# Kernel optimization log

Hardware: AMD Instinct MI355X
Metric: run time of the kernel (lower is better)

The kernel has to match this reference:

```python
import jax, jax.numpy as jnp
import numpy as np

N = 100000   # nodes
E = 1600000  # edges (avg degree 16)
D_IN = 128
HID = [128, 128]
D_OUT = 1


def _linear_params(key, in_c, out_c):
    k1, k2 = jax.random.split(key)
    s = 1.0 / np.sqrt(in_c)
    w = jax.random.uniform(k1, (out_c, in_c), jnp.float32, -s, s)
    b = jax.random.uniform(k2, (out_c,), jnp.float32, -s, s)
    return w, b


def setup_inputs() -> dict:
    key = jax.random.key(0)
    ks = jax.random.split(key, 16)
    inp = {}
    inp["x"] = jax.random.normal(ks[0], (N, D_IN), jnp.float32)
    inp["edge_index"] = jax.random.randint(ks[1], (2, E), 0, N, jnp.int32)
    # 3 GINConvs: dims (128->128), (128->128), (128->128); each MLP = Linear, ReLU, Linear
    dims = [(D_IN, HID[0]), (HID[0], HID[1]), (HID[1], HID[1])]
    for i, (ic, oc) in enumerate(dims):
        k1, k2 = jax.random.split(ks[2 + i])
        w1, b1 = _linear_params(k1, ic, oc)
        w2, b2 = _linear_params(k2, oc, oc)
        inp[f"c{i}_w1"], inp[f"c{i}_b1"] = w1, b1
        inp[f"c{i}_w2"], inp[f"c{i}_b2"] = w2, b2
        inp[f"c{i}_eps"] = jnp.zeros((), jnp.float32)  # train_eps=True, init 0
    last = HID[-1]
    inp["fc1_w"], inp["fc1_b"] = _linear_params(ks[8], last, last // 2)
    inp["fc2_w"], inp["fc2_b"] = _linear_params(ks[9], last // 2, D_OUT)
    return inp


def reference(x, edge_index,
              c0_w1, c0_b1, c0_w2, c0_b2, c0_eps,
              c1_w1, c1_b1, c1_w2, c1_b2, c1_eps,
              c2_w1, c2_b1, c2_w2, c2_b2, c2_eps,
              fc1_w, fc1_b, fc2_w, fc2_b):
    src, dst = edge_index[0], edge_index[1]  # messages flow src -> dst
    n = x.shape[0]

    def gin_conv(h, w1, b1, w2, b2, eps):
        # sum-aggregate neighbor features: scatter-add h[src] into dst
        agg = jax.ops.segment_sum(h[src], dst, num_segments=n)
        z = (1.0 + eps) * h + agg
        z = jax.nn.relu(z @ w1.T + b1) @ w2.T + b2  # GIN MLP
        return jax.nn.relu(z)  # outer ReLU in GINNet.forward

    h = gin_conv(x, c0_w1, c0_b1, c0_w2, c0_b2, c0_eps)
    h = gin_conv(h, c1_w1, c1_b1, c1_w2, c1_b2, c1_eps)
    h = gin_conv(h, c2_w1, c2_b1, c2_w2, c2_b2, c2_eps)
    h = jax.nn.relu(h @ fc1_w.T + fc1_b)
    return jax.nn.sigmoid(h @ fc2_w.T + fc2_b)
```

## Files before the change

### kernel.cpp

```cpp
#include <hip/hip_runtime.h>
#include <math.h>


using f16   = _Float16;
using f16x4 = __attribute__((ext_vector_type(4))) _Float16;
using f16x8 = __attribute__((ext_vector_type(8))) _Float16;
using f32x4 = __attribute__((ext_vector_type(4))) float;

constexpr int BINBLK = 256;

__device__ inline void glds16(const void* g, void* l) {
    __builtin_amdgcn_global_load_lds(
        (const __attribute__((address_space(1))) void*)g,
        (__attribute__((address_space(3))) void*)l, 16, 0, 0);
}


__global__ __launch_bounds__(512) void bucket_count_kernel(const int* __restrict__ dst,
                                                           int* __restrict__ cntM,
                                                           int E, int nbuck) {
    __shared__ int cnt[512];
    for (int i = threadIdx.x; i < nbuck; i += 512) cnt[i] = 0;
    __syncthreads();
    int chunk = (E + gridDim.x - 1) / gridDim.x;
    int lo = blockIdx.x * chunk, hi = min(lo + chunk, E);
    for (int e = lo + threadIdx.x; e < hi; e += 512)
        atomicAdd(&cnt[dst[e] >> 8], 1);
    __syncthreads();
    for (int i = threadIdx.x; i < nbuck; i += 512)
        cntM[(size_t)i * gridDim.x + blockIdx.x] = cnt[i];
}

__global__ __launch_bounds__(256) void scan_partial(const int* __restrict__ deg,
                                                    int* __restrict__ bsum, int n) {
    __shared__ int red[256];
    int b = blockIdx.x, t = threadIdx.x;
    int base = b * 1024;
    int s = 0;
#pragma unroll
    for (int j = 0; j < 4; ++j) {
        int idx = base + j * 256 + t;
        if (idx < n) s += deg[idx];
    }
    red[t] = s;
    __syncthreads();
    for (int d = 128; d > 0; d >>= 1) {
        if (t < d) red[t] += red[t + d];
        __syncthreads();
    }
    if (t == 0) bsum[b] = red[0];
}

__global__ __launch_bounds__(128) void scan_bsum(const int* __restrict__ bsum,
                                                 int* __restrict__ bbase, int nb,
                                                 int* __restrict__ total_out) {
    __shared__ int s[128];
    int t = threadIdx.x;
    s[t] = (t < nb) ? bsum[t] : 0;
    __syncthreads();
    for (int d = 1; d < 128; d <<= 1) {
        int v = (t >= d) ? s[t - d] : 0;
        __syncthreads();
        s[t] += v;
        __syncthreads();
    }
    bbase[t] = (t > 0) ? s[t - 1] : 0;
    if (t == 127) total_out[0] = s[127];
}

__global__ __launch_bounds__(256) void scan_final(const int* __restrict__ deg,
                                                  const int* __restrict__ bbase,
                                                  int* __restrict__ outA,
                                                  int* __restrict__ outB, int n) {
    __shared__ int red[256];
    int b = blockIdx.x, t = threadIdx.x;
    int base = b * 1024 + t * 4;
    int d0 = 0, d1 = 0, d2 = 0, d3 = 0;
    if (base + 3 < n) {
        int4 v = *(const int4*)&deg[base];
        d0 = v.x; d1 = v.y; d2 = v.z; d3 = v.w;
    } else {
        if (base < n) d0 = deg[base];
        if (base + 1 < n) d1 = deg[base + 1];
        if (base + 2 < n) d2 = deg[base + 2];
    }
    red[t] = d0 + d1 + d2 + d3;
    __syncthreads();
    for (int d = 1; d < 256; d <<= 1) {
        int v = (t >= d) ? red[t - d] : 0;
        __syncthreads();
        red[t] += v;
        __syncthreads();
    }
    int ex = bbase[b] + ((t > 0) ? red[t - 1] : 0);
    int o0 = ex, o1 = ex + d0, o2 = o1 + d1, o3 = o2 + d2;
    if (base + 3 < n) {
        *(int4*)&outA[base] = make_int4(o0, o1, o2, o3);
        *(int4*)&outB[base] = make_int4(o0, o1, o2, o3);
    } else {
        if (base < n) { outA[base] = o0; outB[base] = o0; }
        if (base + 1 < n) { outA[base + 1] = o1; outB[base + 1] = o1; }
        if (base + 2 < n) { outA[base + 2] = o2; outB[base + 2] = o2; }
    }
}

__global__ __launch_bounds__(512) void bin_kernel(const int* __restrict__ src,
                                                  const int* __restrict__ dst,
                                                  const int* __restrict__ baseM,
                                                  int2* __restrict__ stage, int E, int nbuck) {
    __shared__ int cur[512];
    for (int i = threadIdx.x; i < nbuck; i += 512)
        cur[i] = baseM[(size_t)i * gridDim.x + blockIdx.x];
    __syncthreads();
    int chunk = (E + gridDim.x - 1) / gridDim.x;
    int lo = blockIdx.x * chunk, hi = min(lo + chunk, E);
    for (int e = lo + threadIdx.x; e < hi; e += 512) {
        int d = dst[e];
        int p = atomicAdd(&cur[d >> 8], 1);
        stage[p] = make_int2(src[e], d);
    }
}

__global__ __launch_bounds__(256) void csr_kernel(const int2* __restrict__ stage,
                                                  const int* __restrict__ baseM,
                                                  int* __restrict__ offs,
                                                  int* __restrict__ col,
                                                  int E, int N, int nbuck, int binblk) {
    constexpr int CAP = 10240;
    __shared__ int cnt[256];
    __shared__ int sc[256];
    __shared__ int colbuf[CAP];
    int b = blockIdx.x, t = threadIdx.x;
    int base = baseM[(size_t)b * binblk];
    int end = (b + 1 < nbuck) ? baseM[(size_t)(b + 1) * binblk] : E;
    cnt[t] = 0;
    __syncthreads();
    for (int e = base + t; e < end; e += 256)
        atomicAdd(&cnt[stage[e].y & 255], 1);
    __syncthreads();
    int myCnt = cnt[t];
    sc[t] = myCnt;
    __syncthreads();
    for (int d = 1; d < 256; d <<= 1) {
        int u = (t >= d) ? sc[t - d] : 0;
        __syncthreads();
        sc[t] += u;
        __syncthreads();
    }
    int myExcl = sc[t] - myCnt;
    int node = b * 256 + t;
    if (node <= N) offs[node] = base + myExcl;
    cnt[t] = myExcl;
    __syncthreads();
    for (int e = base + t; e < end; e += 256) {
        int2 sd = stage[e];
        int p = atomicAdd(&cnt[sd.y & 255], 1);
        if (p < CAP) colbuf[p] = sd.x;
        else col[base + p] = sd.x;
    }
    __syncthreads();
    int lim = min(end - base, CAP);
    for (int i = t; i < lim; i += 256) col[base + i] = colbuf[i];
}

__global__ void cvt4_kernel(const float* __restrict__ in, f16* __restrict__ out, int nq) {
    int stride = gridDim.x * blockDim.x;
    for (int i = blockIdx.x * blockDim.x + threadIdx.x; i < nq; i += stride) {
        float4 v = *(const float4*)(in + (size_t)i * 4);
        f16x4 o = {(f16)v.x, (f16)v.y, (f16)v.z, (f16)v.w};
        *(f16x4*)(out + (size_t)i * 4) = o;
    }
}

struct CvtPack {
    const float* s[7];
    f16* d[7];
    int nq[7];
};
__global__ void cvt_pack_kernel(CvtPack p) {
    int seg = blockIdx.y;
    int nq = p.nq[seg];
    const float* in = p.s[seg];
    f16* out = p.d[seg];
    int stride = gridDim.x * blockDim.x;
    for (int i = blockIdx.x * blockDim.x + threadIdx.x; i < nq; i += stride) {
        float4 v = *(const float4*)(in + (size_t)i * 4);
        f16x4 o = {(f16)v.x, (f16)v.y, (f16)v.z, (f16)v.w};
        *(f16x4*)(out + (size_t)i * 4) = o;
    }
}

__global__ __launch_bounds__(256) void agg_kernel(const f16* __restrict__ h,
                                                  const int* __restrict__ offs,
                                                  const int* __restrict__ col,
                                                  const float* __restrict__ epsp,
                                                  f16* __restrict__ z, int n) {
    int node = blockIdx.x * 8 + (threadIdx.x >> 5);
    int li = threadIdx.x & 31;
    bool valid = node < n;
    int nd = valid ? node : (n - 1);
    const f16x4* hp = (const f16x4*)h;
    float e1 = 1.0f + epsp[0];
    f16x4 self = hp[(size_t)nd * 32 + li];
    float a0 = (float)self.x * e1, a1 = (float)self.y * e1;
    float a2 = (float)self.z * e1, a3 = (float)self.w * e1;
    int lo = offs[nd], hi = valid ? offs[nd + 1] : lo;

    int e = lo;
    for (; e + 8 <= hi; e += 8) {
        int idx[8];
#pragma unroll
        for (int j = 0; j < 8; ++j) idx[j] = col[e + j];
        f16x4 v[8];
#pragma unroll
        for (int j = 0; j < 8; ++j) v[j] = hp[(size_t)idx[j] * 32 + li];
#pragma unroll
        for (int j = 0; j < 8; ++j) {
            a0 += (float)v[j].x; a1 += (float)v[j].y;
            a2 += (float)v[j].z; a3 += (float)v[j].w;
        }
    }
    if (e + 4 <= hi) {
        int idx[4];
#pragma unroll
        for (int j = 0; j < 4; ++j) idx[j] = col[e + j];
        f16x4 v[4];
#pragma unroll
        for (int j = 0; j < 4; ++j) v[j] = hp[(size_t)idx[j] * 32 + li];
#pragma unroll
        for (int j = 0; j < 4; ++j) {
            a0 += (float)v[j].x; a1 += (float)v[j].y;
            a2 += (float)v[j].z; a3 += (float)v[j].w;
        }
        e += 4;
    }
    for (; e < hi; ++e) {
        f16x4 v = hp[(size_t)col[e] * 32 + li];
        a0 += (float)v.x; a1 += (float)v.y; a2 += (float)v.z; a3 += (float)v.w;
    }
    if (valid) {
        f16x4 o = {(f16)a0, (f16)a1, (f16)a2, (f16)a3};
        __builtin_nontemporal_store(o, (f16x4*)z + (size_t)nd * 32 + li);
    }
}

template <bool LAST>
__global__ __launch_bounds__(256) void conv_mlp_kernel(
    const f16* __restrict__ Z, const f16* __restrict__ W1f,
    const float* __restrict__ b1, const f16* __restrict__ W2f,
    const float* __restrict__ b2, f16* __restrict__ Hout, int M,
    const f16* __restrict__ fc1wf, const float* __restrict__ fc1b,
    const float* __restrict__ fc2w, const float* __restrict__ fc2b,
    float* __restrict__ out) {
    __shared__ __align__(16) f16 As[128 * 128];
    __shared__ __align__(16) f16 Ws[128 * 128];
    __shared__ float Red[LAST ? 128 * 17 : 1];

    const int tid = threadIdx.x;
    const int w = tid >> 6, lane = tid & 63;
    const int frow = lane & 15, kgrp = lane >> 4;
    const int m0 = blockIdx.x * 128;
    const int u = lane & 15, rsub = lane >> 4;

#pragma unroll
    for (int i = 0; i < 8; ++i) {
        int rowbase = (w * 8 + i) * 4;
        int r = rowbase + rsub;
        int gr = m0 + r;
        if (gr >= M) gr = M - 1;
        glds16(Z + (size_t)gr * 128 + ((u ^ (r & 7)) << 3), &As[rowbase * 128]);
    }
#pragma unroll
    for (int i = 0; i < 8; ++i) {
        int rowbase = (w * 8 + i) * 4;
        int r = rowbase + rsub;
        glds16(W1f + (size_t)r * 128 + ((u ^ (r & 7)) << 3), &Ws[rowbase * 128]);
    }
    __syncthreads();

    const int arow0 = w * 32 + frow;
    f32x4 acc[2][8];
#pragma unroll
    for (int mi = 0; mi < 2; ++mi)
#pragma unroll
        for (int nj = 0; nj < 8; ++nj) acc[mi][nj] = (f32x4){0.f, 0.f, 0.f, 0.f};

#pragma unroll
    for (int kk = 0; kk < 4; ++kk) {
        int kb = kk * 4 + kgrp;
        f16x8 a[2], b[8];
#pragma unroll
        for (int mi = 0; mi < 2; ++mi) {
            int r = arow0 + mi * 16;
            a[mi] = *(const f16x8*)&As[r * 128 + ((kb ^ (r & 7)) << 3)];
        }
#pragma unroll
        for (int nj = 0; nj < 8; ++nj) {
            int r = nj * 16 + frow;
            b[nj] = *(const f16x8*)&Ws[r * 128 + ((kb ^ (r & 7)) << 3)];
        }
#pragma unroll
        for (int mi = 0; mi < 2; ++mi)
#pragma unroll
            for (int nj = 0; nj < 8; ++nj)
                acc[mi][nj] = __builtin_amdgcn_mfma_f32_16x16x32_f16(a[mi], b[nj],
                                                                     acc[mi][nj], 0, 0, 0);
    }
    __syncthreads();

#pragma unroll
    for (int i = 0; i < 8; ++i) {
        int rowbase = (w * 8 + i) * 4;
        int r = rowbase + rsub;
        glds16(W2f + (size_t)r * 128 + ((u ^ (r & 7)) << 3), &Ws[rowbase * 128]);
    }
    {
        float bv[8];
#pragma unroll
        for (int nj = 0; nj < 8; ++nj) bv[nj] = b1[nj * 16 + frow];
#pragma unroll
        for (int mi = 0; mi < 2; ++mi)
#pragma unroll
            for (int nj = 0; nj < 8; ++nj) {
                int row0 = w * 32 + mi * 16 + kgrp * 4;
                int c = nj * 16 + frow;
                int cu = c >> 3, cl = c & 7;
#pragma unroll
                for (int r = 0; r < 4; ++r) {
                    int rr = row0 + r;
                    As[rr * 128 + ((cu ^ (rr & 7)) << 3) + cl] =
                        (f16)fmaxf(acc[mi][nj][r] + bv[nj], 0.f);
                }
            }
    }
    __syncthreads();

#pragma unroll
    for (int mi = 0; mi < 2; ++mi)
#pragma unroll
        for (int nj = 0; nj < 8; ++nj) acc[mi][nj] = (f32x4){0.f, 0.f, 0.f, 0.f};
#pragma unroll
    for (int kk = 0; kk < 4; ++kk) {
        int kb = kk * 4 + kgrp;
        f16x8 a[2], b[8];
#pragma unroll
        for (int mi = 0; mi < 2; ++mi) {
            int r = arow0 + mi * 16;
            a[mi] = *(const f16x8*)&As[r * 128 + ((kb ^ (r & 7)) << 3)];
        }
#pragma unroll
        for (int nj = 0; nj < 8; ++nj) {
            int r = nj * 16 + frow;
            b[nj] = *(const f16x8*)&Ws[r * 128 + ((kb ^ (r & 7)) << 3)];
        }
#pragma unroll
        for (int mi = 0; mi < 2; ++mi)
#pragma unroll
            for (int nj = 0; nj < 8; ++nj)
                acc[mi][nj] = __builtin_amdgcn_mfma_f32_16x16x32_f16(a[mi], b[nj],
                                                                     acc[mi][nj], 0, 0, 0);
    }

    float bv2[8];
#pragma unroll
    for (int nj = 0; nj < 8; ++nj) bv2[nj] = b2[nj * 16 + frow];

    if (!LAST) {
        __syncthreads();
#pragma unroll
        for (int mi = 0; mi < 2; ++mi)
#pragma unroll
            for (int nj = 0; nj < 8; ++nj) {
                int row0 = w * 32 + mi * 16 + kgrp * 4;
                int c = nj * 16 + frow;
#pragma unroll
                for (int r = 0; r < 4; ++r)
                    As[(row0 + r) * 128 + c] = (f16)fmaxf(acc[mi][nj][r] + bv2[nj], 0.f);
            }
        __syncthreads();
        for (int idx = tid; idx < 128 * 16; idx += 256) {
            int r = idx >> 4, q = idx & 15;
            int gm = m0 + r;
            if (gm < M)
                *(float4*)(Hout + (size_t)gm * 128 + q * 8) = *(const float4*)&As[r * 128 + q * 8];
        }
    } else {
        __syncthreads();
#pragma unroll
        for (int i = 0; i < 4; ++i) {
            int rowbase = (w * 4 + i) * 4;
            int r = rowbase + rsub;
            glds16(fc1wf + (size_t)r * 128 + ((u ^ (r & 7)) << 3), &Ws[rowbase * 128]);
        }
#pragma unroll
        for (int mi = 0; mi < 2; ++mi)
#pragma unroll
            for (int nj = 0; nj < 8; ++nj) {
                int row0 = w * 32 + mi * 16 + kgrp * 4;
                int c = nj * 16 + frow;
                int cu = c >> 3, cl = c & 7;
#pragma unroll
                for (int r = 0; r < 4; ++r) {
                    int rr = row0 + r;
                    As[rr * 128 + ((cu ^ (rr & 7)) << 3) + cl] =
                        (f16)fmaxf(acc[mi][nj][r] + bv2[nj], 0.f);
                }
            }
        __syncthreads();

        f32x4 acc3[2][4];
#pragma unroll
        for (int mi = 0; mi < 2; ++mi)
#pragma unroll
            for (int nj = 0; nj < 4; ++nj) acc3[mi][nj] = (f32x4){0.f, 0.f, 0.f, 0.f};
#pragma unroll
        for (int kk = 0; kk < 4; ++kk) {
            int kb = kk * 4 + kgrp;
            f16x8 a[2], b[4];
#pragma unroll
            for (int mi = 0; mi < 2; ++mi) {
                int r = arow0 + mi * 16;
                a[mi] = *(const f16x8*)&As[r * 128 + ((kb ^ (r & 7)) << 3)];
            }
#pragma unroll
            for (int nj = 0; nj < 4; ++nj) {
                int r = nj * 16 + frow;
                b[nj] = *(const f16x8*)&Ws[r * 128 + ((kb ^ (r & 7)) << 3)];
            }
#pragma unroll
            for (int mi = 0; mi < 2; ++mi)
#pragma unroll
                for (int nj = 0; nj < 4; ++nj)
                    acc3[mi][nj] = __builtin_amdgcn_mfma_f32_16x16x32_f16(a[mi], b[nj],
                                                                          acc3[mi][nj], 0, 0, 0);
        }
        float bvf[4], f2[4];
#pragma unroll
        for (int nj = 0; nj < 4; ++nj) {
            bvf[nj] = fc1b[nj * 16 + frow];
            f2[nj] = fc2w[nj * 16 + frow];
        }
        float part[2][4];
#pragma unroll
        for (int mi = 0; mi < 2; ++mi)
#pragma unroll
            for (int r = 0; r < 4; ++r) part[mi][r] = 0.f;
#pragma unroll
        for (int mi = 0; mi < 2; ++mi)
#pragma unroll
            for (int nj = 0; nj < 4; ++nj)
#pragma unroll
                for (int r = 0; r < 4; ++r)
                    part[mi][r] += fmaxf(acc3[mi][nj][r] + bvf[nj], 0.f) * f2[nj];
#pragma unroll
        for (int mi = 0; mi < 2; ++mi)
#pragma unroll
            for (int r = 0; r < 4; ++r)
                Red[(w * 32 + mi * 16 + kgrp * 4 + r) * 17 + frow] = part[mi][r];
        __syncthreads();
        if (tid < 128) {
            float s = fc2b[0];
#pragma unroll
            for (int q = 0; q < 16; ++q) s += Red[tid * 17 + q];
            int m = m0 + tid;
            if (m < M) out[m] = 1.f / (1.f + expf(-s));
        }
    }
}

extern "C" void kernel_launch(void* const* d_in, const int* in_sizes, int n_in,
                              void* d_out, int out_size, void* d_ws, size_t ws_size,
                              hipStream_t stream) {
    const float* x = (const float*)d_in[0];
    const int* ei = (const int*)d_in[1];
    const int N = in_sizes[0] / 128;
    const int E = in_sizes[1] / 2;
    const int* srcIdx = ei;
    const int* dstIdx = ei + E;

    const float* w1[3] = {(const float*)d_in[2], (const float*)d_in[7], (const float*)d_in[12]};
    const float* b1[3] = {(const float*)d_in[3], (const float*)d_in[8], (const float*)d_in[13]};
    const float* w2[3] = {(const float*)d_in[4], (const float*)d_in[9], (const float*)d_in[14]};
    const float* b2[3] = {(const float*)d_in[5], (const float*)d_in[10], (const float*)d_in[15]};
    const float* eps[3] = {(const float*)d_in[6], (const float*)d_in[11], (const float*)d_in[16]};
    const float* fc1w = (const float*)d_in[17];
    const float* fc1b = (const float*)d_in[18];
    const float* fc2w = (const float*)d_in[19];
    const float* fc2b = (const float*)d_in[20];

    char* ws = (char*)d_ws;
    size_t p = 0;
    auto carve = [&](size_t bytes) -> char* {
        char* r = ws + p;
        p = (p + bytes + 255) & ~(size_t)255;
        return r;
    };
    const int nbuck = (N + 255) >> 8;
    const int nm = nbuck * BINBLK;
    int* offs = (int*)carve((size_t)(N + 1) * 4);
    int* col = (int*)carve((size_t)E * 4);
    int* cntM = (int*)carve((size_t)nm * 4);
    int* baseM = (int*)carve((size_t)nm * 4);
    int* baseM2 = (int*)carve((size_t)nm * 4);
    int* bsum = (int*)carve(128 * 4);
    int* bbase = (int*)carve(128 * 4);
    int* tot = (int*)carve(4);
    int2* stage = (int2*)carve((size_t)E * 8);
    f16* H0 = (f16*)carve((size_t)N * 128 * 2);
    f16* H1 = (f16*)carve((size_t)N * 128 * 2);
    f16* Z = (f16*)carve((size_t)N * 128 * 2);
    f16* w1f[3], *w2f[3];
    for (int i = 0; i < 3; ++i) {
        w1f[i] = (f16*)carve(128 * 128 * 2);
        w2f[i] = (f16*)carve(128 * 128 * 2);
    }
    f16* fc1wf = (f16*)carve(64 * 128 * 2);
    (void)ws_size;

    const int SB2 = (nm + 1023) / 1024;
    bucket_count_kernel<<<BINBLK, 512, 0, stream>>>(dstIdx, cntM, E, nbuck);
    scan_partial<<<SB2, 256, 0, stream>>>(cntM, bsum, nm);
    scan_bsum<<<1, 128, 0, stream>>>(bsum, bbase, SB2, tot);
    scan_final<<<SB2, 256, 0, stream>>>(cntM, bbase, baseM, baseM2, nm);
    bin_kernel<<<BINBLK, 512, 0, stream>>>(srcIdx, dstIdx, baseM, stage, E, nbuck);
    csr_kernel<<<nbuck, 256, 0, stream>>>(stage, baseM, offs, col, E, N, nbuck, BINBLK);

    cvt4_kernel<<<2048, 256, 0, stream>>>(x, H0, N * 128 / 4);
    CvtPack cp;
    for (int i = 0; i < 3; ++i) {
        cp.s[i] = w1[i];     cp.d[i] = w1f[i];     cp.nq[i] = 128 * 128 / 4;
        cp.s[3 + i] = w2[i]; cp.d[3 + i] = w2f[i]; cp.nq[3 + i] = 128 * 128 / 4;
    }
    cp.s[6] = fc1w; cp.d[6] = fc1wf; cp.nq[6] = 64 * 128 / 4;
    cvt_pack_kernel<<<dim3(16, 7), 256, 0, stream>>>(cp);

    const int aggGrid = (N + 7) / 8;
    const int gemmGrid = (N + 127) / 128;

    agg_kernel<<<aggGrid, 256, 0, stream>>>(H0, offs, col, eps[0], Z, N);
    conv_mlp_kernel<false><<<gemmGrid, 256, 0, stream>>>(
        Z, w1f[0], b1[0], w2f[0], b2[0], H1, N, nullptr, nullptr, nullptr, nullptr, nullptr);
    agg_kernel<<<aggGrid, 256, 0, stream>>>(H1, offs, col, eps[1], Z, N);
    conv_mlp_kernel<false><<<gemmGrid, 256, 0, stream>>>(
        Z, w1f[1], b1[1], w2f[1], b2[1], H0, N, nullptr, nullptr, nullptr, nullptr, nullptr);
    agg_kernel<<<aggGrid, 256, 0, stream>>>(H0, offs, col, eps[2], Z, N);
    conv_mlp_kernel<true><<<gemmGrid, 256, 0, stream>>>(
        Z, w1f[2], b1[2], w2f[2], b2[2], nullptr, N, fc1wf, fc1b, fc2w, fc2b, (float*)d_out);
}
```

Measured before the change: 299.9 us.

## Fuse neighbor aggregation into GIN MLP kernel with LDS-staged CSR columns

Removes the separate aggregation kernel and the Z intermediate buffer. Each 512-thread block now gathers and sums neighbor features for its 128 nodes directly into shared memory, then runs the two-layer MLP on that tile. Nodes are handed out to 8-lane groups through a shared-memory atomic counter for load balance. The block's CSR column slice is staged in LDS when it fits, and each wave now computes 16 rows instead of 32. This saves the Z write and read plus launch overhead, at the cost of higher LDS use per block and the gather no longer overlapping with the GEMM phase across blocks.

```diff
diff --git a/kernel.cpp b/kernel.cpp
--- a/kernel.cpp
+++ b/kernel.cpp
@@ -190,71 +190,24 @@
     }
 }
 
-__global__ __launch_bounds__(256) void agg_kernel(const f16* __restrict__ h,
-                                                  const int* __restrict__ offs,
-                                                  const int* __restrict__ col,
-                                                  const float* __restrict__ epsp,
-                                                  f16* __restrict__ z, int n) {
-    int node = blockIdx.x * 8 + (threadIdx.x >> 5);
-    int li = threadIdx.x & 31;
-    bool valid = node < n;
-    int nd = valid ? node : (n - 1);
-    const f16x4* hp = (const f16x4*)h;
-    float e1 = 1.0f + epsp[0];
-    f16x4 self = hp[(size_t)nd * 32 + li];
-    float a0 = (float)self.x * e1, a1 = (float)self.y * e1;
-    float a2 = (float)self.z * e1, a3 = (float)self.w * e1;
-    int lo = offs[nd], hi = valid ? offs[nd + 1] : lo;
-
-    int e = lo;
-    for (; e + 8 <= hi; e += 8) {
-        int idx[8];
-#pragma unroll
-        for (int j = 0; j < 8; ++j) idx[j] = col[e + j];
-        f16x4 v[8];
-#pragma unroll
-        for (int j = 0; j < 8; ++j) v[j] = hp[(size_t)idx[j] * 32 + li];
-#pragma unroll
-        for (int j = 0; j < 8; ++j) {
-            a0 += (float)v[j].x; a1 += (float)v[j].y;
-            a2 += (float)v[j].z; a3 += (float)v[j].w;
-        }
-    }
-    if (e + 4 <= hi) {
-        int idx[4];
-#pragma unroll
-        for (int j = 0; j < 4; ++j) idx[j] = col[e + j];
-        f16x4 v[4];
-#pragma unroll
-        for (int j = 0; j < 4; ++j) v[j] = hp[(size_t)idx[j] * 32 + li];
-#pragma unroll
-        for (int j = 0; j < 4; ++j) {
-            a0 += (float)v[j].x; a1 += (float)v[j].y;
-            a2 += (float)v[j].z; a3 += (float)v[j].w;
-        }
-        e += 4;
-    }
-    for (; e < hi; ++e) {
-        f16x4 v = hp[(size_t)col[e] * 32 + li];
-        a0 += (float)v.x; a1 += (float)v.y; a2 += (float)v.z; a3 += (float)v.w;
-    }
-    if (valid) {
-        f16x4 o = {(f16)a0, (f16)a1, (f16)a2, (f16)a3};
-        __builtin_nontemporal_store(o, (f16x4*)z + (size_t)nd * 32 + li);
-    }
-}
-
 template <bool LAST>
-__global__ __launch_bounds__(256) void conv_mlp_kernel(
-    const f16* __restrict__ Z, const f16* __restrict__ W1f,
-    const float* __restrict__ b1, const f16* __restrict__ W2f,
-    const float* __restrict__ b2, f16* __restrict__ Hout, int M,
+__global__ __launch_bounds__(512, 4) void conv_fused_kernel(
+    const f16* __restrict__ H, const int* __restrict__ offs,
+    const int* __restrict__ col, const float* __restrict__ epsp,
+    const f16* __restrict__ W1f, const float* __restrict__ b1,
+    const f16* __restrict__ W2f, const float* __restrict__ b2,
+    f16* __restrict__ Hout, int M,
     const f16* __restrict__ fc1wf, const float* __restrict__ fc1b,
     const float* __restrict__ fc2w, const float* __restrict__ fc2b,
     float* __restrict__ out) {
+    constexpr int COLCAP = 2560;
     __shared__ __align__(16) f16 As[128 * 128];
     __shared__ __align__(16) f16 Ws[128 * 128];
-    __shared__ float Red[LAST ? 128 * 17 : 1];
+    __shared__ __align__(16) int poolB[COLCAP + 132];
+    int* colLDS = poolB;
+    int* sOffs = poolB + COLCAP;
+    int* ctr = poolB + COLCAP + 130;
+    float* Red = (float*)poolB;
 
     const int tid = threadIdx.x;
     const int w = tid >> 6, lane = tid & 63;
@@ -263,54 +216,116 @@
     const int u = lane & 15, rsub = lane >> 4;
 
 #pragma unroll
-    for (int i = 0; i < 8; ++i) {
-        int rowbase = (w * 8 + i) * 4;
-        int r = rowbase + rsub;
-        int gr = m0 + r;
-        if (gr >= M) gr = M - 1;
-        glds16(Z + (size_t)gr * 128 + ((u ^ (r & 7)) << 3), &As[rowbase * 128]);
-    }
-#pragma unroll
-    for (int i = 0; i < 8; ++i) {
-        int rowbase = (w * 8 + i) * 4;
+    for (int i = 0; i < 4; ++i) {
+        int rowbase = (w * 4 + i) * 4;
         int r = rowbase + rsub;
         glds16(W1f + (size_t)r * 128 + ((u ^ (r & 7)) << 3), &Ws[rowbase * 128]);
     }
-    __syncthreads();
-
-    const int arow0 = w * 32 + frow;
-    f32x4 acc[2][8];
-#pragma unroll
-    for (int mi = 0; mi < 2; ++mi)
-#pragma unroll
-        for (int nj = 0; nj < 8; ++nj) acc[mi][nj] = (f32x4){0.f, 0.f, 0.f, 0.f};
-
+    for (int i = tid; i < 129; i += 512) sOffs[i] = offs[min(m0 + i, M)];
+    if (tid == 0) *ctr = 0;
+    __syncthreads();
+    const int cbase = sOffs[0];
+    const int wlen = sOffs[128] - cbase;
+    const bool useLds = wlen <= COLCAP;
+    if (useLds)
+        for (int i = tid; i < wlen; i += 512)
+            colLDS[i] = __builtin_nontemporal_load(&col[cbase + i]);
+    __syncthreads();
+
+    {
+        const int li = tid & 7;
+        const int gbase = lane & ~7;
+        const f16x8* hp = (const f16x8*)H;
+        const float e1 = 1.0f + epsp[0];
+        for (;;) {
+            int n = 0;
+            if (li == 0) n = atomicAdd(ctr, 1);
+            n = __shfl(n, gbase, 64);
+            if (n >= 128) break;
+            const int coA = li, coB = li + 8;
+            f16* dstA = &As[n * 128 + ((coA ^ (n & 7)) << 3)];
+            f16* dstB = &As[n * 128 + ((coB ^ (n & 7)) << 3)];
+            const int node = m0 + n;
+            if (node >= M) {
+                f16x8 zz = {};
+                *(f16x8*)dstA = zz;
+                *(f16x8*)dstB = zz;
+                continue;
+            }
+            f16x8 sA = hp[(size_t)node * 16 + coA];
+            f16x8 sB = hp[(size_t)node * 16 + coB];
+            float a[8], b[8];
+#pragma unroll
+            for (int c = 0; c < 8; ++c) {
+                a[c] = (float)sA[c] * e1;
+                b[c] = (float)sB[c] * e1;
+            }
+            int lo = sOffs[n] - cbase, hi = sOffs[n + 1] - cbase;
+            int e = lo;
+            for (; e + 6 <= hi; e += 6) {
+                int idx[6];
+#pragma unroll
+                for (int j = 0; j < 6; ++j)
+                    idx[j] = useLds ? colLDS[e + j] : col[cbase + e + j];
+                f16x8 vA[6], vB[6];
+#pragma unroll
+                for (int j = 0; j < 6; ++j) {
+                    vA[j] = hp[(size_t)idx[j] * 16 + coA];
+                    vB[j] = hp[(size_t)idx[j] * 16 + coB];
+                }
+#pragma unroll
+                for (int j = 0; j < 6; ++j)
+#pragma unroll
+                    for (int c = 0; c < 8; ++c) {
+                        a[c] += (float)vA[j][c];
+                        b[c] += (float)vB[j][c];
+                    }
+            }
+            for (; e < hi; ++e) {
+                int idx = useLds ? colLDS[e] : col[cbase + e];
+                f16x8 vA = hp[(size_t)idx * 16 + coA];
+                f16x8 vB = hp[(size_t)idx * 16 + coB];
+#pragma unroll
+                for (int c = 0; c < 8; ++c) {
+                    a[c] += (float)vA[c];
+                    b[c] += (float)vB[c];
+                }
+            }
+            f16x8 oA, oB;
+#pragma unroll
+            for (int c = 0; c < 8; ++c) {
+                oA[c] = (f16)a[c];
+                oB[c] = (f16)b[c];
+            }
+            *(f16x8*)dstA = oA;
+            *(f16x8*)dstB = oB;
+        }
+    }
+    __syncthreads();
+
+    const int arow0 = w * 16 + frow;
+    f32x4 acc[8];
+#pragma unroll
+    for (int nj = 0; nj < 8; ++nj) acc[nj] = (f32x4){0.f, 0.f, 0.f, 0.f};
 #pragma unroll
     for (int kk = 0; kk < 4; ++kk) {
         int kb = kk * 4 + kgrp;
-        f16x8 a[2], b[8];
-#pragma unroll
-        for (int mi = 0; mi < 2; ++mi) {
-            int r = arow0 + mi * 16;
-            a[mi] = *(const f16x8*)&As[r * 128 + ((kb ^ (r & 7)) << 3)];
-        }
+        f16x8 a = *(const f16x8*)&As[arow0 * 128 + ((kb ^ (arow0 & 7)) << 3)];
+        f16x8 b[8];
 #pragma unroll
         for (int nj = 0; nj < 8; ++nj) {
             int r = nj * 16 + frow;
             b[nj] = *(const f16x8*)&Ws[r * 128 + ((kb ^ (r & 7)) << 3)];
         }
 #pragma unroll
-        for (int mi = 0; mi < 2; ++mi)
-#pragma unroll
-            for (int nj = 0; nj < 8; ++nj)
-                acc[mi][nj] = __builtin_amdgcn_mfma_f32_16x16x32_f16(a[mi], b[nj],
-                                                                     acc[mi][nj], 0, 0, 0);
-    }
-    __syncthreads();
-
-#pragma unroll
-    for (int i = 0; i < 8; ++i) {
-        int rowbase = (w * 8 + i) * 4;
+        for (int nj = 0; nj < 8; ++nj)
+            acc[nj] = __builtin_amdgcn_mfma_f32_16x16x32_f16(a, b[nj], acc[nj], 0, 0, 0);
+    }
+    __syncthreads();
+
+#pragma unroll
+    for (int i = 0; i < 4; ++i) {
+        int rowbase = (w * 4 + i) * 4;
         int r = rowbase + rsub;
         glds16(W2f + (size_t)r * 128 + ((u ^ (r & 7)) << 3), &Ws[rowbase * 128]);
     }
@@ -318,67 +333,53 @@
         float bv[8];
 #pragma unroll
         for (int nj = 0; nj < 8; ++nj) bv[nj] = b1[nj * 16 + frow];
-#pragma unroll
-        for (int mi = 0; mi < 2; ++mi)
-#pragma unroll
-            for (int nj = 0; nj < 8; ++nj) {
-                int row0 = w * 32 + mi * 16 + kgrp * 4;
-                int c = nj * 16 + frow;
-                int cu = c >> 3, cl = c & 7;
-#pragma unroll
-                for (int r = 0; r < 4; ++r) {
-                    int rr = row0 + r;
-                    As[rr * 128 + ((cu ^ (rr & 7)) << 3) + cl] =
-                        (f16)fmaxf(acc[mi][nj][r] + bv[nj], 0.f);
-                }
-            }
-    }
-    __syncthreads();
-
-#pragma unroll
-    for (int mi = 0; mi < 2; ++mi)
-#pragma unroll
-        for (int nj = 0; nj < 8; ++nj) acc[mi][nj] = (f32x4){0.f, 0.f, 0.f, 0.f};
+        const int row0 = w * 16 + kgrp * 4;
+#pragma unroll
+        for (int nj = 0; nj < 8; ++nj) {
+            int c = nj * 16 + frow;
+            int cu = c >> 3, cl = c & 7;
+#pragma unroll
+            for (int r = 0; r < 4; ++r) {
+                int rr = row0 + r;
+                As[rr * 128 + ((cu ^ (rr & 7)) << 3) + cl] =
+                    (f16)fmaxf(acc[nj][r] + bv[nj], 0.f);
+            }
+        }
+    }
+    __syncthreads();
+
+#pragma unroll
+    for (int nj = 0; nj < 8; ++nj) acc[nj] = (f32x4){0.f, 0.f, 0.f, 0.f};
 #pragma unroll
     for (int kk = 0; kk < 4; ++kk) {
         int kb = kk * 4 + kgrp;
-        f16x8 a[2], b[8];
-#pragma unroll
-        for (int mi = 0; mi < 2; ++mi) {
-            int r = arow0 + mi * 16;
-            a[mi] = *(const f16x8*)&As[r * 128 + ((kb ^ (r & 7)) << 3)];
-        }
+        f16x8 a = *(const f16x8*)&As[arow0 * 128 + ((kb ^ (arow0 & 7)) << 3)];
+        f16x8 b[8];
 #pragma unroll
         for (int nj = 0; nj < 8; ++nj) {
             int r = nj * 16 + frow;
             b[nj] = *(const f16x8*)&Ws[r * 128 + ((kb ^ (r & 7)) << 3)];
         }
 #pragma unroll
-        for (int mi = 0; mi < 2; ++mi)
-#pragma unroll
-            for (int nj = 0; nj < 8; ++nj)
-                acc[mi][nj] = __builtin_amdgcn_mfma_f32_16x16x32_f16(a[mi], b[nj],
-                                                                     acc[mi][nj], 0, 0, 0);
-    }
-
+        for (int nj = 0; nj < 8; ++nj)
+            acc[nj] = __builtin_amdgcn_mfma_f32_16x16x32_f16(a, b[nj], acc[nj], 0, 0, 0);
+    }
     float bv2[8];
 #pragma unroll
     for (int nj = 0; nj < 8; ++nj) bv2[nj] = b2[nj * 16 + frow];
 
     if (!LAST) {
         __syncthreads();
-#pragma unroll
-        for (int mi = 0; mi < 2; ++mi)
-#pragma unroll
-            for (int nj = 0; nj < 8; ++nj) {
-                int row0 = w * 32 + mi * 16 + kgrp * 4;
-                int c = nj * 16 + frow;
-#pragma unroll
-                for (int r = 0; r < 4; ++r)
-                    As[(row0 + r) * 128 + c] = (f16)fmaxf(acc[mi][nj][r] + bv2[nj], 0.f);
-            }
-        __syncthreads();
-        for (int idx = tid; idx < 128 * 16; idx += 256) {
+        const int row0 = w * 16 + kgrp * 4;
+#pragma unroll
+        for (int nj = 0; nj < 8; ++nj) {
+            int c = nj * 16 + frow;
+#pragma unroll
+            for (int r = 0; r < 4; ++r)
+                As[(row0 + r) * 128 + c] = (f16)fmaxf(acc[nj][r] + bv2[nj], 0.f);
+        }
+        __syncthreads();
+        for (int idx = tid; idx < 128 * 16; idx += 512) {
             int r = idx >> 4, q = idx & 15;
             int gm = m0 + r;
             if (gm < M)
@@ -387,52 +388,41 @@
     } else {
         __syncthreads();
 #pragma unroll
-        for (int i = 0; i < 4; ++i) {
-            int rowbase = (w * 4 + i) * 4;
+        for (int i = 0; i < 2; ++i) {
+            int rowbase = (w * 2 + i) * 4;
             int r = rowbase + rsub;
             glds16(fc1wf + (size_t)r * 128 + ((u ^ (r & 7)) << 3), &Ws[rowbase * 128]);
         }
-#pragma unroll
-        for (int mi = 0; mi < 2; ++mi)
-#pragma unroll
-            for (int nj = 0; nj < 8; ++nj) {
-                int row0 = w * 32 + mi * 16 + kgrp * 4;
-                int c = nj * 16 + frow;
-                int cu = c >> 3, cl = c & 7;
-#pragma unroll
-                for (int r = 0; r < 4; ++r) {
-                    int rr = row0 + r;
-                    As[rr * 128 + ((cu ^ (rr & 7)) << 3) + cl] =
-                        (f16)fmaxf(acc[mi][nj][r] + bv2[nj], 0.f);
-                }
-            }
-        __syncthreads();
-
-        f32x4 acc3[2][4];
-#pragma unroll
-        for (int mi = 0; mi < 2; ++mi)
-#pragma unroll
-            for (int nj = 0; nj < 4; ++nj) acc3[mi][nj] = (f32x4){0.f, 0.f, 0.f, 0.f};
+        const int row0 = w * 16 + kgrp * 4;
+#pragma unroll
+        for (int nj = 0; nj < 8; ++nj) {
+            int c = nj * 16 + frow;
+            int cu = c >> 3, cl = c & 7;
+#pragma unroll
+            for (int r = 0; r < 4; ++r) {
+                int rr = row0 + r;
+                As[rr * 128 + ((cu ^ (rr & 7)) << 3) + cl] =
+                    (f16)fmaxf(acc[nj][r] + bv2[nj], 0.f);
+            }
+        }
+        __syncthreads();
+
+        f32x4 acc3[4];
+#pragma unroll
+        for (int nj = 0; nj < 4; ++nj) acc3[nj] = (f32x4){0.f, 0.f, 0.f, 0.f};
 #pragma unroll
         for (int kk = 0; kk < 4; ++kk) {
             int kb = kk * 4 + kgrp;
-            f16x8 a[2], b[4];
-#pragma unroll
-            for (int mi = 0; mi < 2; ++mi) {
-                int r = arow0 + mi * 16;
-                a[mi] = *(const f16x8*)&As[r * 128 + ((kb ^ (r & 7)) << 3)];
-            }
+            f16x8 a = *(const f16x8*)&As[arow0 * 128 + ((kb ^ (arow0 & 7)) << 3)];
+            f16x8 b[4];
 #pragma unroll
             for (int nj = 0; nj < 4; ++nj) {
                 int r = nj * 16 + frow;
                 b[nj] = *(const f16x8*)&Ws[r * 128 + ((kb ^ (r & 7)) << 3)];
             }
 #pragma unroll
-            for (int mi = 0; mi < 2; ++mi)
-#pragma unroll
-                for (int nj = 0; nj < 4; ++nj)
-                    acc3[mi][nj] = __builtin_amdgcn_mfma_f32_16x16x32_f16(a[mi], b[nj],
-                                                                          acc3[mi][nj], 0, 0, 0);
+            for (int nj = 0; nj < 4; ++nj)
+                acc3[nj] = __builtin_amdgcn_mfma_f32_16x16x32_f16(a, b[nj], acc3[nj], 0, 0, 0);
         }
         float bvf[4], f2[4];
 #pragma unroll
@@ -440,23 +430,14 @@
             bvf[nj] = fc1b[nj * 16 + frow];
             f2[nj] = fc2w[nj * 16 + frow];
         }
-        float part[2][4];
-#pragma unroll
-        for (int mi = 0; mi < 2; ++mi)
-#pragma unroll
-            for (int r = 0; r < 4; ++r) part[mi][r] = 0.f;
-#pragma unroll
-        for (int mi = 0; mi < 2; ++mi)
-#pragma unroll
-            for (int nj = 0; nj < 4; ++nj)
-#pragma unroll
-                for (int r = 0; r < 4; ++r)
-                    part[mi][r] += fmaxf(acc3[mi][nj][r] + bvf[nj], 0.f) * f2[nj];
-#pragma unroll
-        for (int mi = 0; mi < 2; ++mi)
+        float part[4] = {0.f, 0.f, 0.f, 0.f};
+#pragma unroll
+        for (int nj = 0; nj < 4; ++nj)
 #pragma unroll
             for (int r = 0; r < 4; ++r)
-                Red[(w * 32 + mi * 16 + kgrp * 4 + r) * 17 + frow] = part[mi][r];
+                part[r] += fmaxf(acc3[nj][r] + bvf[nj], 0.f) * f2[nj];
+#pragma unroll
+        for (int r = 0; r < 4; ++r) Red[(row0 + r) * 17 + frow] = part[r];
         __syncthreads();
         if (tid < 128) {
             float s = fc2b[0];
@@ -508,7 +489,6 @@
     int2* stage = (int2*)carve((size_t)E * 8);
     f16* H0 = (f16*)carve((size_t)N * 128 * 2);
     f16* H1 = (f16*)carve((size_t)N * 128 * 2);
-    f16* Z = (f16*)carve((size_t)N * 128 * 2);
     f16* w1f[3], *w2f[3];
     for (int i = 0; i < 3; ++i) {
         w1f[i] = (f16*)carve(128 * 128 * 2);
@@ -534,16 +514,15 @@
     cp.s[6] = fc1w; cp.d[6] = fc1wf; cp.nq[6] = 64 * 128 / 4;
     cvt_pack_kernel<<<dim3(16, 7), 256, 0, stream>>>(cp);
 
-    const int aggGrid = (N + 7) / 8;
     const int gemmGrid = (N + 127) / 128;
 
-    agg_kernel<<<aggGrid, 256, 0, stream>>>(H0, offs, col, eps[0], Z, N);
-    conv_mlp_kernel<false><<<gemmGrid, 256, 0, stream>>>(
-        Z, w1f[0], b1[0], w2f[0], b2[0], H1, N, nullptr, nullptr, nullptr, nullptr, nullptr);
-    agg_kernel<<<aggGrid, 256, 0, stream>>>(H1, offs, col, eps[1], Z, N);
-    conv_mlp_kernel<false><<<gemmGrid, 256, 0, stream>>>(
-        Z, w1f[1], b1[1], w2f[1], b2[1], H0, N, nullptr, nullptr, nullptr, nullptr, nullptr);
-    agg_kernel<<<aggGrid, 256, 0, stream>>>(H0, offs, col, eps[2], Z, N);
-    conv_mlp_kernel<true><<<gemmGrid, 256, 0, stream>>>(
-        Z, w1f[2], b1[2], w2f[2], b2[2], nullptr, N, fc1wf, fc1b, fc2w, fc2b, (float*)d_out);
-}
+    conv_fused_kernel<false><<<gemmGrid, 512, 0, stream>>>(
+        H0, offs, col, eps[0], w1f[0], b1[0], w2f[0], b2[0], H1, N,
+        nullptr, nullptr, nullptr, nullptr, nullptr);
+    conv_fused_kernel<false><<<gemmGrid, 512, 0, stream>>>(
+        H1, offs, col, eps[1], w1f[1], b1[1], w2f[1], b2[1], H0, N,
+        nullptr, nullptr, nullptr, nullptr, nullptr);
+    conv_fused_kernel<true><<<gemmGrid, 512, 0, stream>>>(
+        H0, offs, col, eps[2], w1f[2], b1[2], w2f[2], b2[2], nullptr, N,
+        fc1wf, fc1b, fc2w, fc2b, (float*)d_out);
+}
```

Result: slower. 315.6 us (+5.2%).

## Restructure aggregation with LDS-staged column indices and shrink CSR staging

Applied to the files above, without the earlier changes.

The aggregation kernel now processes 128 nodes per block. It preloads the block's column indices into LDS and hands nodes to 8-lane groups through an LDS atomic counter, with each lane loading 16-byte f16x8 vectors. The aim is to cut repeated global index loads, balance work across nodes of different degree, and widen the gather loads. The CSR build also packs src and the low dst byte into one int, which halves staging traffic, and drops the duplicate baseM2 output. The packing assumes source indices fit in 24 bits, and the dynamic counter adds some atomic overhead.

```diff
diff --git a/kernel.cpp b/kernel.cpp
--- a/kernel.cpp
+++ b/kernel.cpp
@@ -70,8 +70,7 @@
 
 __global__ __launch_bounds__(256) void scan_final(const int* __restrict__ deg,
                                                   const int* __restrict__ bbase,
-                                                  int* __restrict__ outA,
-                                                  int* __restrict__ outB, int n) {
+                                                  int* __restrict__ outA, int n) {
     __shared__ int red[256];
     int b = blockIdx.x, t = threadIdx.x;
     int base = b * 1024 + t * 4;
@@ -96,18 +95,17 @@
     int o0 = ex, o1 = ex + d0, o2 = o1 + d1, o3 = o2 + d2;
     if (base + 3 < n) {
         *(int4*)&outA[base] = make_int4(o0, o1, o2, o3);
-        *(int4*)&outB[base] = make_int4(o0, o1, o2, o3);
     } else {
-        if (base < n) { outA[base] = o0; outB[base] = o0; }
-        if (base + 1 < n) { outA[base + 1] = o1; outB[base + 1] = o1; }
-        if (base + 2 < n) { outA[base + 2] = o2; outB[base + 2] = o2; }
+        if (base < n) outA[base] = o0;
+        if (base + 1 < n) outA[base + 1] = o1;
+        if (base + 2 < n) outA[base + 2] = o2;
     }
 }
 
 __global__ __launch_bounds__(512) void bin_kernel(const int* __restrict__ src,
                                                   const int* __restrict__ dst,
                                                   const int* __restrict__ baseM,
-                                                  int2* __restrict__ stage, int E, int nbuck) {
+                                                  int* __restrict__ stage, int E, int nbuck) {
     __shared__ int cur[512];
     for (int i = threadIdx.x; i < nbuck; i += 512)
         cur[i] = baseM[(size_t)i * gridDim.x + blockIdx.x];
@@ -117,11 +115,11 @@
     for (int e = lo + threadIdx.x; e < hi; e += 512) {
         int d = dst[e];
         int p = atomicAdd(&cur[d >> 8], 1);
-        stage[p] = make_int2(src[e], d);
-    }
-}
-
-__global__ __launch_bounds__(256) void csr_kernel(const int2* __restrict__ stage,
+        stage[p] = (src[e] << 8) | (d & 255);
+    }
+}
+
+__global__ __launch_bounds__(256) void csr_kernel(const int* __restrict__ stage,
                                                   const int* __restrict__ baseM,
                                                   int* __restrict__ offs,
                                                   int* __restrict__ col,
@@ -136,7 +134,7 @@
     cnt[t] = 0;
     __syncthreads();
     for (int e = base + t; e < end; e += 256)
-        atomicAdd(&cnt[stage[e].y & 255], 1);
+        atomicAdd(&cnt[stage[e] & 255], 1);
     __syncthreads();
     int myCnt = cnt[t];
     sc[t] = myCnt;
@@ -153,10 +151,10 @@
     cnt[t] = myExcl;
     __syncthreads();
     for (int e = base + t; e < end; e += 256) {
-        int2 sd = stage[e];
-        int p = atomicAdd(&cnt[sd.y & 255], 1);
-        if (p < CAP) colbuf[p] = sd.x;
-        else col[base + p] = sd.x;
+        int sd = stage[e];
+        int p = atomicAdd(&cnt[sd & 255], 1);
+        if (p < CAP) colbuf[p] = sd >> 8;
+        else col[base + p] = sd >> 8;
     }
     __syncthreads();
     int lim = min(end - base, CAP);
@@ -195,52 +193,83 @@
                                                   const int* __restrict__ col,
                                                   const float* __restrict__ epsp,
                                                   f16* __restrict__ z, int n) {
-    int node = blockIdx.x * 8 + (threadIdx.x >> 5);
-    int li = threadIdx.x & 31;
-    bool valid = node < n;
-    int nd = valid ? node : (n - 1);
-    const f16x4* hp = (const f16x4*)h;
-    float e1 = 1.0f + epsp[0];
-    f16x4 self = hp[(size_t)nd * 32 + li];
-    float a0 = (float)self.x * e1, a1 = (float)self.y * e1;
-    float a2 = (float)self.z * e1, a3 = (float)self.w * e1;
-    int lo = offs[nd], hi = valid ? offs[nd + 1] : lo;
-
-    int e = lo;
-    for (; e + 8 <= hi; e += 8) {
-        int idx[8];
-#pragma unroll
-        for (int j = 0; j < 8; ++j) idx[j] = col[e + j];
-        f16x4 v[8];
-#pragma unroll
-        for (int j = 0; j < 8; ++j) v[j] = hp[(size_t)idx[j] * 32 + li];
-#pragma unroll
-        for (int j = 0; j < 8; ++j) {
-            a0 += (float)v[j].x; a1 += (float)v[j].y;
-            a2 += (float)v[j].z; a3 += (float)v[j].w;
-        }
-    }
-    if (e + 4 <= hi) {
-        int idx[4];
-#pragma unroll
-        for (int j = 0; j < 4; ++j) idx[j] = col[e + j];
-        f16x4 v[4];
-#pragma unroll
-        for (int j = 0; j < 4; ++j) v[j] = hp[(size_t)idx[j] * 32 + li];
-#pragma unroll
-        for (int j = 0; j < 4; ++j) {
-            a0 += (float)v[j].x; a1 += (float)v[j].y;
-            a2 += (float)v[j].z; a3 += (float)v[j].w;
-        }
-        e += 4;
-    }
-    for (; e < hi; ++e) {
-        f16x4 v = hp[(size_t)col[e] * 32 + li];
-        a0 += (float)v.x; a1 += (float)v.y; a2 += (float)v.z; a3 += (float)v.w;
-    }
-    if (valid) {
-        f16x4 o = {(f16)a0, (f16)a1, (f16)a2, (f16)a3};
-        __builtin_nontemporal_store(o, (f16x4*)z + (size_t)nd * 32 + li);
+    constexpr int COLCAP = 3072;
+    __shared__ int colLDS[COLCAP];
+    __shared__ int sOffs[129];
+    __shared__ int ctr;
+    const int tid = threadIdx.x;
+    const int nb = blockIdx.x * 128;
+    for (int i = tid; i < 129; i += 256) sOffs[i] = offs[min(nb + i, n)];
+    if (tid == 0) ctr = 0;
+    __syncthreads();
+    const int base = sOffs[0];
+    const int wlen = sOffs[128] - base;
+    const bool useLds = wlen <= COLCAP;
+    if (useLds)
+        for (int i = tid; i < wlen; i += 256)
+            colLDS[i] = __builtin_nontemporal_load(&col[base + i]);
+    __syncthreads();
+
+    const int li = tid & 7;
+    const int gbase = (tid & 63) & ~7;
+    const f16x8* hp = (const f16x8*)h;
+    const float e1 = 1.0f + epsp[0];
+
+    for (;;) {
+        int m = 0;
+        if (li == 0) m = atomicAdd(&ctr, 1);
+        m = __shfl(m, gbase, 64);
+        if (m >= 128) break;
+        const int node = nb + m;
+        if (node >= n) break;
+        const int coA = li, coB = li + 8;
+        f16x8 sA = hp[(size_t)node * 16 + coA];
+        f16x8 sB = hp[(size_t)node * 16 + coB];
+        float a[8], b[8];
+#pragma unroll
+        for (int c = 0; c < 8; ++c) {
+            a[c] = (float)sA[c] * e1;
+            b[c] = (float)sB[c] * e1;
+        }
+        int lo = sOffs[m] - base, hi = sOffs[m + 1] - base;
+        int e = lo;
+        for (; e + 6 <= hi; e += 6) {
+            int idx[6];
+#pragma unroll
+            for (int j = 0; j < 6; ++j)
+                idx[j] = useLds ? colLDS[e + j] : col[base + e + j];
+            f16x8 vA[6], vB[6];
+#pragma unroll
+            for (int j = 0; j < 6; ++j) {
+                vA[j] = hp[(size_t)idx[j] * 16 + coA];
+                vB[j] = hp[(size_t)idx[j] * 16 + coB];
+            }
+#pragma unroll
+            for (int j = 0; j < 6; ++j)
+#pragma unroll
+                for (int c = 0; c < 8; ++c) {
+                    a[c] += (float)vA[j][c];
+                    b[c] += (float)vB[j][c];
+                }
+        }
+        for (; e < hi; ++e) {
+            int idx = useLds ? colLDS[e] : col[base + e];
+            f16x8 vA = hp[(size_t)idx * 16 + coA];
+            f16x8 vB = hp[(size_t)idx * 16 + coB];
+#pragma unroll
+            for (int c = 0; c < 8; ++c) {
+                a[c] += (float)vA[c];
+                b[c] += (float)vB[c];
+            }
+        }
+        f16x8 oA, oB;
+#pragma unroll
+        for (int c = 0; c < 8; ++c) {
+            oA[c] = (f16)a[c];
+            oB[c] = (f16)b[c];
+        }
+        __builtin_nontemporal_store(oA, (f16x8*)z + (size_t)node * 16 + coA);
+        __builtin_nontemporal_store(oB, (f16x8*)z + (size_t)node * 16 + coB);
     }
 }
 
@@ -501,11 +530,10 @@
     int* col = (int*)carve((size_t)E * 4);
     int* cntM = (int*)carve((size_t)nm * 4);
     int* baseM = (int*)carve((size_t)nm * 4);
-    int* baseM2 = (int*)carve((size_t)nm * 4);
     int* bsum = (int*)carve(128 * 4);
     int* bbase = (int*)carve(128 * 4);
     int* tot = (int*)carve(4);
-    int2* stage = (int2*)carve((size_t)E * 8);
+    int* stage = (int*)carve((size_t)E * 4);
     f16* H0 = (f16*)carve((size_t)N * 128 * 2);
     f16* H1 = (f16*)carve((size_t)N * 128 * 2);
     f16* Z = (f16*)carve((size_t)N * 128 * 2);
@@ -521,7 +549,7 @@
     bucket_count_kernel<<<BINBLK, 512, 0, stream>>>(dstIdx, cntM, E, nbuck);
     scan_partial<<<SB2, 256, 0, stream>>>(cntM, bsum, nm);
     scan_bsum<<<1, 128, 0, stream>>>(bsum, bbase, SB2, tot);
-    scan_final<<<SB2, 256, 0, stream>>>(cntM, bbase, baseM, baseM2, nm);
+    scan_final<<<SB2, 256, 0, stream>>>(cntM, bbase, baseM, nm);
     bin_kernel<<<BINBLK, 512, 0, stream>>>(srcIdx, dstIdx, baseM, stage, E, nbuck);
     csr_kernel<<<nbuck, 256, 0, stream>>>(stage, baseM, offs, col, E, N, nbuck, BINBLK);
 
@@ -534,7 +562,7 @@
     cp.s[6] = fc1w; cp.d[6] = fc1wf; cp.nq[6] = 64 * 128 / 4;
     cvt_pack_kernel<<<dim3(16, 7), 256, 0, stream>>>(cp);
 
-    const int aggGrid = (N + 7) / 8;
+    const int aggGrid = (N + 127) / 128;
     const int gemmGrid = (N + 127) / 128;
 
     agg_kernel<<<aggGrid, 256, 0, stream>>>(H0, offs, col, eps[0], Z, N);
```

After: 346.0 us. +15.4%, slower.
